# Kernel optimization log

Measured on AMD Instinct MI355X. Metric: run time of the kernel, lower is better.

Reference implementation:

```python
import jax, jax.numpy as jnp
import numpy as np

N_NODES = 20000
N_EDGES = 320000
N_GRAPHS = 64
IN_FEAT = 64
HIDDEN = 256
GRID = 4
NUM_LAYERS = 4  # -> 3 Fourier message-passing layers
NEG_SLOPE = 0.01  # nn.LeakyReLU default


def setup_inputs() -> dict:
    key = jax.random.key(0)
    ks = jax.random.split(key, 8)
    h = jax.random.normal(ks[0], (N_NODES, IN_FEAT), dtype=jnp.float32)
    src = jax.random.randint(ks[1], (N_EDGES,), 0, N_NODES, dtype=jnp.int32)
    dst = jax.random.randint(ks[2], (N_EDGES,), 0, N_NODES, dtype=jnp.int32)
    graph_ids = jnp.sort(jax.random.randint(ks[3], (N_NODES,), 0, N_GRAPHS, dtype=jnp.int32))
    # KAN_polynomial(in_feat, hidden, degree=grid_feat), init randn/(sqrt(in)*sqrt(deg))
    W_line = jax.random.normal(ks[4], (HIDDEN, IN_FEAT, GRID + 1), dtype=jnp.float32) / (
        np.sqrt(IN_FEAT) * np.sqrt(GRID))
    # 3 NaiveFourierKANLayer coeffs [2, out, in, grid]
    fourier_coeffs = jax.random.normal(ks[5], (NUM_LAYERS - 1, 2, HIDDEN, HIDDEN, GRID),
                                       dtype=jnp.float32) / (np.sqrt(HIDDEN) * np.sqrt(GRID))
    # Readout KAN_polynomial(hidden, 1, degree=1, addbias=True)
    W_out = jax.random.normal(ks[6], (1, HIDDEN, 2), dtype=jnp.float32) / np.sqrt(HIDDEN)
    b_out = jnp.zeros((1, 1), dtype=jnp.float32)
    return {"h": h, "src": src, "dst": dst, "graph_ids": graph_ids,
            "W_line": W_line, "fourier_coeffs": fourier_coeffs,
            "W_out": W_out, "b_out": b_out}


def kan_polynomial(x, coeffs, bias=None):
    # x: [b, in], coeffs: [out, in, deg+1]
    deg = coeffs.shape[-1] - 1
    powers = jnp.stack([x ** i for i in range(deg + 1)], axis=-1)  # [b, in, deg+1]
    y = jnp.einsum('bid,oid->bo', powers, coeffs)
    if bias is not None:
        y = y + bias
    return y


def fourier_kan(x, coeffs):
    # x: [N, in], coeffs: [2, out, in, grid]
    grid = coeffs.shape[-1]
    k = jnp.arange(1, grid + 1, dtype=x.dtype)  # [grid]
    ang = x[:, :, None] * k  # [N, in, grid]
    y = jnp.einsum('nig,oig->no', jnp.cos(ang), coeffs[0])
    y = y + jnp.einsum('nig,oig->no', jnp.sin(ang), coeffs[1])
    return y


def reference(h, src, dst, graph_ids, W_line, fourier_coeffs, W_out, b_out):
    # kan_line
    h = kan_polynomial(h, W_line)  # [N, hidden]
    # message-passing Fourier KAN layers with residual + leaky_relu
    for l in range(NUM_LAYERS - 1):
        agg = jax.ops.segment_sum(h[src], dst, num_segments=N_NODES)  # copy_u + sum
        m = fourier_kan(agg, fourier_coeffs[l])
        h = jax.nn.leaky_relu(m + h, negative_slope=NEG_SLOPE)
    # avg pooling per graph
    sums = jax.ops.segment_sum(h, graph_ids, num_segments=N_GRAPHS)  # [G, hidden]
    counts = jax.ops.segment_sum(jnp.ones((N_NODES,), dtype=h.dtype), graph_ids,
                                 num_segments=N_GRAPHS)
    y = sums / jnp.maximum(counts, 1.0)[:, None]
    # Readout: KAN_polynomial(hidden, 1, degree=1) + sigmoid
    out = jax.nn.sigmoid(kan_polynomial(y, W_out, b_out))  # [G, 1]
    return out
```

## Files before the change

kernel.cpp:

```cpp
#include <hip/hip_runtime.h>
#include <math.h>

#define N_NODES   20000
#define N_PAD2    20096
#define N_EDGES   320000
#define N_GRAPHS  64
#define IN_FEAT   64
#define HIDDEN    256
#define GRID_F    4
#define NLAYERS   3
#define NEG_SLOPE 0.01f

#define KF 2048
#define KL4 256
#define NB_SCAN 79
#define NRG  157
#define NBLK (NRG * 4)
#define NLBLK 1256

typedef _Float16 f16x8 __attribute__((ext_vector_type(8)));
typedef _Float16 f16x2 __attribute__((ext_vector_type(2)));
typedef float    f32x4 __attribute__((ext_vector_type(4)));

__global__ void transpose_fourier_f16(const float* __restrict__ fc, _Float16* __restrict__ Bt) {
    int idx = blockIdx.x * 256 + threadIdx.x;
    int kk  = idx & 2047;
    int rest = idx >> 11;
    int o = rest & 255;
    int l = rest >> 8;
    int i = kk >> 3, f = kk & 7, g = f >> 1, t = f & 1;
    Bt[idx] = (_Float16)fc[(((size_t)(l * 2 + t) * HIDDEN + o) * HIDDEN + i) * GRID_F + g];
}

__global__ void transpose_line4(const float* __restrict__ wl, _Float16* __restrict__ Wth,
                                _Float16* __restrict__ Wtl) {
    int idx = blockIdx.x * 256 + threadIdx.x;
    int o = idx >> 8, kk = idx & 255;
    int i = kk >> 2, d = (kk & 3) + 1;
    float wv = wl[(o * IN_FEAT + i) * 5 + d];
    _Float16 h = (_Float16)wv;
    Wth[idx] = h;
    Wtl[idx] = (_Float16)(wv - (float)h);
}

__global__ void line_bias(const float* __restrict__ wl, float* __restrict__ biasv) {
    int o = threadIdx.x;
    float s = 0.f;
    for (int i = 0; i < IN_FEAT; ++i) s += wl[(o * IN_FEAT + i) * 5];
    biasv[o] = s;
}

__global__ void count_deg(const int* __restrict__ dst, int* __restrict__ counts) {
    int e = blockIdx.x * 256 + threadIdx.x;
    if (e < N_EDGES) atomicAdd(&counts[dst[e]], 1);
}

__global__ void block_sums(const int* __restrict__ counts, int* __restrict__ bsum) {
    int i = blockIdx.x * 256 + threadIdx.x;
    int v = (i < N_NODES) ? counts[i] : 0;
    #pragma unroll
    for (int o = 32; o > 0; o >>= 1) v += __shfl_down(v, o, 64);
    __shared__ int ws[4];
    if ((threadIdx.x & 63) == 0) ws[threadIdx.x >> 6] = v;
    __syncthreads();
    if (threadIdx.x == 0) bsum[blockIdx.x] = ws[0] + ws[1] + ws[2] + ws[3];
}

__global__ void scan_mid(const int* __restrict__ bsum, int* __restrict__ bofs,
                         int* __restrict__ row_start) {
    __shared__ int buf[128];
    int t = threadIdx.x;
    int v = (t < NB_SCAN) ? bsum[t] : 0;
    buf[t] = v;
    __syncthreads();
    for (int d = 1; d < 128; d <<= 1) {
        int x = (t >= d) ? buf[t - d] : 0;
        __syncthreads();
        buf[t] += x;
        __syncthreads();
    }
    if (t < NB_SCAN) bofs[t] = buf[t] - v;
    if (t == NB_SCAN - 1) row_start[N_NODES] = buf[t];
}

__global__ void scan_blocks(const int* __restrict__ counts, const int* __restrict__ bofs,
                            int* __restrict__ row_start) {
    int i = blockIdx.x * 256 + threadIdx.x;
    int val = (i < N_NODES) ? counts[i] : 0;
    int lane = threadIdx.x & 63, wid = threadIdx.x >> 6;
    int v = val;
    #pragma unroll
    for (int d = 1; d < 64; d <<= 1) {
        int t = __shfl_up(v, d, 64);
        if (lane >= d) v += t;
    }
    __shared__ int ws[4];
    if (lane == 63) ws[wid] = v;
    __syncthreads();
    int wofs = 0;
    for (int j = 0; j < wid; ++j) wofs += ws[j];
    if (i < N_NODES) row_start[i] = bofs[blockIdx.x] + wofs + v - val;
}

__global__ void fill_csr(const int* __restrict__ src, const int* __restrict__ dst,
                         const int* __restrict__ row_start, int* __restrict__ cursor,
                         int* __restrict__ ssrc) {
    int e = blockIdx.x * 256 + threadIdx.x;
    if (e < N_EDGES) {
        int d = dst[e];
        int pos = row_start[d] + atomicAdd(&cursor[d], 1);
        ssrc[pos] = src[e];
    }
}

__global__ __launch_bounds__(256)
void aggregate(const float* __restrict__ h, const int* __restrict__ row_start,
               const int* __restrict__ ssrc, unsigned* __restrict__ cs) {
    const int node = blockIdx.x * 4 + (threadIdx.x >> 6);
    const int lane = threadIdx.x & 63;
    const int b = row_start[node], e = row_start[node + 1];
    f32x4 a0 = {0.f, 0.f, 0.f, 0.f}, a1 = {0.f, 0.f, 0.f, 0.f};
    int j = b;
    for (; j + 1 < e; j += 2) {
        int s0 = ssrc[j], s1 = ssrc[j + 1];
        a0 += *(const f32x4*)&h[(size_t)s0 * HIDDEN + lane * 4];
        a1 += *(const f32x4*)&h[(size_t)s1 * HIDDEN + lane * 4];
    }
    if (j < e) {
        int s0 = ssrc[j];
        a0 += *(const f32x4*)&h[(size_t)s0 * HIDDEN + lane * 4];
    }
    f32x4 v = a0 + a1;
    unsigned csv[4];
    #pragma unroll
    for (int k = 0; k < 4; ++k) {
        float r = v[k] * 0.15915494309189535f;
        r -= floorf(r);
        _Float16 ch = (_Float16)__builtin_amdgcn_cosf(r);
        _Float16 sh = (_Float16)__builtin_amdgcn_sinf(r);
        union { f16x2 z; unsigned u; } p;
        p.z = (f16x2){ch, sh};
        csv[k] = p.u;
    }
    *(uint4*)&cs[(size_t)node * HIDDEN + lane * 4] = make_uint4(csv[0], csv[1], csv[2], csv[3]);
}

__device__ __forceinline__ void makepow(float xa, float xb, f16x8& hi, f16x8& lo) {
    float p0 = xa, p1 = xa * xa;
    float p2 = p1 * xa, p3 = p1 * p1;
    float q0 = xb, q1 = xb * xb;
    float q2 = q1 * xb, q3 = q1 * q1;
    float pp[8] = {p0, p1, p2, p3, q0, q1, q2, q3};
    #pragma unroll
    for (int j = 0; j < 8; ++j) {
        _Float16 h = (_Float16)pp[j];
        hi[j] = h;
        lo[j] = (_Float16)(pp[j] - (float)h);
    }
}

__global__ __launch_bounds__(256)
void kan_line_mfma(const float* __restrict__ x, const _Float16* __restrict__ Wth,
                   const _Float16* __restrict__ Wtl, const float* __restrict__ biasv,
                   float* __restrict__ out) {
    __shared__ float    As[64][64];
    __shared__ _Float16 Bsh[64][136];
    __shared__ _Float16 Bsl[64][136];

    const int t = threadIdx.x;
    const int w = t >> 6, l = t & 63, ln = l & 15, quad = l >> 4;
    const int wr = w >> 1, wc = w & 1;

    const int g   = blockIdx.x;
    const int bid = (g & 7) * 157 + (g >> 3);
    const int Mbase = (bid >> 2) * 64;
    const int col0  = (bid & 3) * 64;

    #pragma unroll
    for (int r = 0; r < 4; ++r) {
        int idx = r * 256 + t;
        int row = idx >> 4, p = idx & 15;
        int grow = Mbase + row;
        if (grow > N_NODES - 1) grow = N_NODES - 1;
        f32x4 v = *(const f32x4*)&x[(size_t)grow * IN_FEAT + p * 4];
        *(f32x4*)&As[row][(p * 4) ^ ((row & 7) << 2)] = v;
    }
    const _Float16* WthB = Wth + (size_t)col0 * KL4;
    const _Float16* WtlB = Wtl + (size_t)col0 * KL4;
    #pragma unroll
    for (int r = 0; r < 4; ++r) {
        int idx = r * 256 + t;
        int c = idx >> 4, p = idx & 15;
        *(f16x8*)&Bsh[c][p * 8] = *(const f16x8*)&WthB[(size_t)c * KL4 + p * 8];
        *(f16x8*)&Bsl[c][p * 8] = *(const f16x8*)&WtlB[(size_t)c * KL4 + p * 8];
    }
    f16x8 pbh[4], pbl[4];
    #pragma unroll
    for (int r = 0; r < 4; ++r) {
        int idx = r * 256 + t;
        int c = idx >> 4, p = idx & 15;
        pbh[r] = *(const f16x8*)&WthB[(size_t)c * KL4 + 128 + p * 8];
        pbl[r] = *(const f16x8*)&WtlB[(size_t)c * KL4 + 128 + p * 8];
    }
    __syncthreads();

    f32x4 acc[2][2];
    #pragma unroll
    for (int rt = 0; rt < 2; ++rt)
        #pragma unroll
        for (int ct = 0; ct < 2; ++ct)
            acc[rt][ct] = (f32x4){0.f, 0.f, 0.f, 0.f};

    const int lr0 = wr * 32 + ln;
    const int xsw = (lr0 & 7) << 2;

    #pragma unroll
    for (int half = 0; half < 2; ++half) {
        #pragma unroll
        for (int kcl = 0; kcl < 4; ++kcl) {
            const int kc = half * 4 + kcl;
            const int f0 = kc * 8 + quad * 2;
            float x00 = As[lr0     ][f0 ^ xsw];
            float x01 = As[lr0     ][(f0 + 1) ^ xsw];
            float x10 = As[lr0 + 16][f0 ^ xsw];
            float x11 = As[lr0 + 16][(f0 + 1) ^ xsw];
            f16x8 ah0, al0, ah1, al1;
            makepow(x00, x01, ah0, al0);
            makepow(x10, x11, ah1, al1);
            #pragma unroll
            for (int ct = 0; ct < 2; ++ct) {
                const int bc = wc * 32 + ct * 16 + ln;
                f16x8 bh = *(const f16x8*)&Bsh[bc][kcl * 32 + quad * 8];
                f16x8 bl = *(const f16x8*)&Bsl[bc][kcl * 32 + quad * 8];
                acc[0][ct] = __builtin_amdgcn_mfma_f32_16x16x32_f16(ah0, bh, acc[0][ct], 0, 0, 0);
                acc[0][ct] = __builtin_amdgcn_mfma_f32_16x16x32_f16(al0, bh, acc[0][ct], 0, 0, 0);
                acc[0][ct] = __builtin_amdgcn_mfma_f32_16x16x32_f16(ah0, bl, acc[0][ct], 0, 0, 0);
                acc[1][ct] = __builtin_amdgcn_mfma_f32_16x16x32_f16(ah1, bh, acc[1][ct], 0, 0, 0);
                acc[1][ct] = __builtin_amdgcn_mfma_f32_16x16x32_f16(al1, bh, acc[1][ct], 0, 0, 0);
                acc[1][ct] = __builtin_amdgcn_mfma_f32_16x16x32_f16(ah1, bl, acc[1][ct], 0, 0, 0);
            }
        }
        if (half == 0) {
            __syncthreads();
            #pragma unroll
            for (int r = 0; r < 4; ++r) {
                int idx = r * 256 + t;
                int c = idx >> 4, p = idx & 15;
                *(f16x8*)&Bsh[c][p * 8] = pbh[r];
                *(f16x8*)&Bsl[c][p * 8] = pbl[r];
            }
            __syncthreads();
        }
    }

    #pragma unroll
    for (int rt = 0; rt < 2; ++rt) {
        const int row0 = Mbase + wr * 32 + rt * 16 + quad * 4;
        #pragma unroll
        for (int ct = 0; ct < 2; ++ct) {
            const int col = col0 + wc * 32 + ct * 16 + ln;
            const float bv = biasv[col];
            #pragma unroll
            for (int r = 0; r < 4; ++r) {
                const int row = row0 + r;
                if (row < N_NODES)
                    out[(size_t)row * HIDDEN + col] = acc[rt][ct][r] + bv;
            }
        }
    }
}

__device__ __forceinline__ f16x8 expand4(unsigned csu) {
    union { unsigned u; f16x2 z; } w; w.u = csu;
    f16x2 z1 = w.z;
    f16x2 cc = {z1[0], z1[0]};
    f16x2 ms = {(_Float16)(-z1[1]), z1[1]};
    f16x2 z2 = z1 * cc + (f16x2){z1[1], z1[0]} * ms;
    f16x2 z3 = z2 * cc + (f16x2){z2[1], z2[0]} * ms;
    f16x2 z4 = z3 * cc + (f16x2){z3[1], z3[0]} * ms;
    union { f16x8 v; f16x2 p[4]; } u;
    u.p[0] = z1; u.p[1] = z2; u.p[2] = z3; u.p[3] = z4;
    return u.v;
}

__global__ __launch_bounds__(256)
void fourier_mfma(const unsigned* __restrict__ cs, float* hio,
                  const _Float16* __restrict__ Bt) {
    __shared__ _Float16 Bs[2][64][140];
    __shared__ unsigned As[2][128][17];

    const int t    = threadIdx.x;
    const int w    = t >> 6;
    const int l    = t & 63;
    const int ln   = l & 15;
    const int quad = l >> 4;

    const int g   = blockIdx.x;
    const int xcd = g & 7, ii = g >> 3;
    const int bid = (xcd < 4 ? xcd * 79 : 316 + (xcd - 4) * 78) + ii;
    const int Mbase = (bid >> 2) * 128;
    const int col0  = (bid & 3) * 64;

    const int sc = t >> 4, sp = t & 15;
    const int sr = t >> 2, sq = t & 3;
    const _Float16* bg0 = Bt + (size_t)(col0 + sc) * KF + sp * 8;
    const _Float16* bg1 = bg0 + (size_t)16 * KF;
    const _Float16* bg2 = bg0 + (size_t)32 * KF;
    const _Float16* bg3 = bg0 + (size_t)48 * KF;
    const unsigned* ag0 = cs + (size_t)(Mbase + sr) * HIDDEN + sq * 4;
    const unsigned* ag1 = ag0 + (size_t)64 * HIDDEN;

    f32x4 acc[2][4];
    #pragma unroll
    for (int rt = 0; rt < 2; ++rt)
        #pragma unroll
        for (int ct = 0; ct < 4; ++ct)
            acc[rt][ct] = (f32x4){0.f, 0.f, 0.f, 0.f};

    f16x8 sb0, sb1, sb2, sb3;
    uint4 sa0, sa1;

    sb0 = *(const f16x8*)(bg0);
    sb1 = *(const f16x8*)(bg1);
    sb2 = *(const f16x8*)(bg2);
    sb3 = *(const f16x8*)(bg3);
    sa0 = *(const uint4*)(ag0);
    sa1 = *(const uint4*)(ag1);
    *(f16x8*)&Bs[0][sc     ][sp * 8] = sb0;
    *(f16x8*)&Bs[0][sc + 16][sp * 8] = sb1;
    *(f16x8*)&Bs[0][sc + 32][sp * 8] = sb2;
    *(f16x8*)&Bs[0][sc + 48][sp * 8] = sb3;
    As[0][sr     ][sq * 4 + 0] = sa0.x;
    As[0][sr     ][sq * 4 + 1] = sa0.y;
    As[0][sr     ][sq * 4 + 2] = sa0.z;
    As[0][sr     ][sq * 4 + 3] = sa0.w;
    As[0][sr + 64][sq * 4 + 0] = sa1.x;
    As[0][sr + 64][sq * 4 + 1] = sa1.y;
    As[0][sr + 64][sq * 4 + 2] = sa1.z;
    As[0][sr + 64][sq * 4 + 3] = sa1.w;
    __syncthreads();

    const int lr0 = w * 32 + ln;

    for (int kg = 0; kg < 16; ++kg) {
        const int b = kg & 1;
        if (kg < 15) {
            sb0 = *(const f16x8*)(bg0 + (kg + 1) * 128);
            sb1 = *(const f16x8*)(bg1 + (kg + 1) * 128);
            sb2 = *(const f16x8*)(bg2 + (kg + 1) * 128);
            sb3 = *(const f16x8*)(bg3 + (kg + 1) * 128);
            sa0 = *(const uint4*)(ag0 + (kg + 1) * 16);
            sa1 = *(const uint4*)(ag1 + (kg + 1) * 16);
        }
        #pragma unroll
        for (int kc = 0; kc < 4; ++kc) {
            unsigned cv0 = As[b][lr0     ][kc * 4 + quad];
            unsigned cv1 = As[b][lr0 + 16][kc * 4 + quad];
            f16x8 b0 = *(const f16x8*)&Bs[b][ln     ][kc * 32 + quad * 8];
            f16x8 b1 = *(const f16x8*)&Bs[b][ln + 16][kc * 32 + quad * 8];
            f16x8 b2 = *(const f16x8*)&Bs[b][ln + 32][kc * 32 + quad * 8];
            f16x8 b3 = *(const f16x8*)&Bs[b][ln + 48][kc * 32 + quad * 8];
            f16x8 a0 = expand4(cv0);
            f16x8 a1 = expand4(cv1);
            acc[0][0] = __builtin_amdgcn_mfma_f32_16x16x32_f16(a0, b0, acc[0][0], 0, 0, 0);
            acc[0][1] = __builtin_amdgcn_mfma_f32_16x16x32_f16(a0, b1, acc[0][1], 0, 0, 0);
            acc[0][2] = __builtin_amdgcn_mfma_f32_16x16x32_f16(a0, b2, acc[0][2], 0, 0, 0);
            acc[0][3] = __builtin_amdgcn_mfma_f32_16x16x32_f16(a0, b3, acc[0][3], 0, 0, 0);
            acc[1][0] = __builtin_amdgcn_mfma_f32_16x16x32_f16(a1, b0, acc[1][0], 0, 0, 0);
            acc[1][1] = __builtin_amdgcn_mfma_f32_16x16x32_f16(a1, b1, acc[1][1], 0, 0, 0);
            acc[1][2] = __builtin_amdgcn_mfma_f32_16x16x32_f16(a1, b2, acc[1][2], 0, 0, 0);
            acc[1][3] = __builtin_amdgcn_mfma_f32_16x16x32_f16(a1, b3, acc[1][3], 0, 0, 0);
        }
        if (kg < 15) {
            const int nb = b ^ 1;
            *(f16x8*)&Bs[nb][sc     ][sp * 8] = sb0;
            *(f16x8*)&Bs[nb][sc + 16][sp * 8] = sb1;
            *(f16x8*)&Bs[nb][sc + 32][sp * 8] = sb2;
            *(f16x8*)&Bs[nb][sc + 48][sp * 8] = sb3;
            As[nb][sr     ][sq * 4 + 0] = sa0.x;
            As[nb][sr     ][sq * 4 + 1] = sa0.y;
            As[nb][sr     ][sq * 4 + 2] = sa0.z;
            As[nb][sr     ][sq * 4 + 3] = sa0.w;
            As[nb][sr + 64][sq * 4 + 0] = sa1.x;
            As[nb][sr + 64][sq * 4 + 1] = sa1.y;
            As[nb][sr + 64][sq * 4 + 2] = sa1.z;
            As[nb][sr + 64][sq * 4 + 3] = sa1.w;
        }
        __syncthreads();
    }

    #pragma unroll
    for (int rt = 0; rt < 2; ++rt) {
        const int row0 = Mbase + w * 32 + rt * 16 + quad * 4;
        #pragma unroll
        for (int ct = 0; ct < 4; ++ct) {
            const int col = col0 + ct * 16 + ln;
            #pragma unroll
            for (int r = 0; r < 4; ++r) {
                const int row = row0 + r;
                if (row < N_NODES) {
                    float v = acc[rt][ct][r] + hio[(size_t)row * HIDDEN + col];
                    v = v > 0.f ? v : NEG_SLOPE * v;
                    hio[(size_t)row * HIDDEN + col] = v;
                }
            }
        }
    }
}

__global__ void graph_bounds(const int* __restrict__ gid, int* __restrict__ gstart) {
    int g = threadIdx.x;
    if (g < N_GRAPHS) {
        int lo = 0, hi = N_NODES;
        while (lo < hi) { int mid = (lo + hi) >> 1; if (gid[mid] < g) lo = mid + 1; else hi = mid; }
        gstart[g] = lo;
    } else if (g == N_GRAPHS) {
        gstart[g] = N_NODES;
    }
}

__global__ __launch_bounds__(256)
void pool_seg(const float* __restrict__ h, const int* __restrict__ gid,
              float* __restrict__ pooled) {
    const int c = threadIdx.x;
    const int s = blockIdx.x * 128;
    const int e = min(s + 128, N_NODES);
    float acc = 0.f;
    int g = gid[s];
    for (int n = s; n < e; ++n) {
        int gn = gid[n];
        if (gn != g) {
            atomicAdd(&pooled[g * HIDDEN + c], acc);
            acc = 0.f;
            g = gn;
        }
        acc += h[(size_t)n * HIDDEN + c];
    }
    atomicAdd(&pooled[g * HIDDEN + c], acc);
}

__global__ void readout(const float* __restrict__ pooled, const int* __restrict__ gstart,
                        const float* __restrict__ wout, const float* __restrict__ bout,
                        float* __restrict__ out) {
    int g = blockIdx.x, t = threadIdx.x;
    float cnt = fmaxf((float)(gstart[g + 1] - gstart[g]), 1.f);
    float y = pooled[g * HIDDEN + t] / cnt;
    float term = wout[t * 2 + 0] + wout[t * 2 + 1] * y;
    #pragma unroll
    for (int o = 32; o > 0; o >>= 1) term += __shfl_down(term, o, 64);
    __shared__ float wsum[4];
    if ((t & 63) == 0) wsum[t >> 6] = term;
    __syncthreads();
    if (t == 0) {
        float s = wsum[0] + wsum[1] + wsum[2] + wsum[3] + bout[0];
        out[g] = 1.f / (1.f + expf(-s));
    }
}

extern "C" void kernel_launch(void* const* d_in, const int* in_sizes, int n_in,
                              void* d_out, int out_size, void* d_ws, size_t ws_size,
                              hipStream_t stream) {
    const float* h_in  = (const float*)d_in[0];
    const int*   src   = (const int*)d_in[1];
    const int*   dst   = (const int*)d_in[2];
    const int*   gid   = (const int*)d_in[3];
    const float* wline = (const float*)d_in[4];
    const float* fcoef = (const float*)d_in[5];
    const float* wout  = (const float*)d_in[6];
    const float* bout  = (const float*)d_in[7];
    float* out = (float*)d_out;

    char* ws = (char*)d_ws;
    size_t off = 0;
    auto alloc = [&](size_t bytes) {
        size_t o = off;
        off += (bytes + 255) & ~size_t(255);
        return o;
    };
    float*     hbuf      = (float*)(ws + alloc((size_t)N_PAD2 * HIDDEN * 4));
    unsigned*  csbuf     = (unsigned*)(ws + alloc((size_t)N_PAD2 * HIDDEN * 4));
    _Float16*  BtF16     = (_Float16*)(ws + alloc((size_t)NLAYERS * KF * HIDDEN * 2));
    _Float16*  Wth       = (_Float16*)(ws + alloc((size_t)HIDDEN * KL4 * 2));
    _Float16*  Wtl       = (_Float16*)(ws + alloc((size_t)HIDDEN * KL4 * 2));
    float*     biasv     = (float*)(ws + alloc((size_t)HIDDEN * 4));
    int*       row_start = (int*)(ws + alloc((size_t)(N_NODES + 1) * 4));
    int*       counts    = (int*)(ws + alloc((size_t)N_NODES * 4));
    int*       cursor    = (int*)(ws + alloc((size_t)N_NODES * 4));
    int*       ssrc      = (int*)(ws + alloc((size_t)N_EDGES * 4));
    int*       bsum      = (int*)(ws + alloc((size_t)128 * 4));
    int*       bofs      = (int*)(ws + alloc((size_t)128 * 4));
    int*       gstart    = (int*)(ws + alloc((size_t)(N_GRAPHS + 1) * 4));
    float*     pooled    = (float*)(ws + alloc((size_t)N_GRAPHS * HIDDEN * 4));

    hipMemsetAsync(counts, 0, (size_t)N_NODES * 4, stream);
    hipMemsetAsync(cursor, 0, (size_t)N_NODES * 4, stream);
    hipMemsetAsync(pooled, 0, (size_t)N_GRAPHS * HIDDEN * 4, stream);
    hipMemsetAsync(csbuf + (size_t)N_NODES * HIDDEN, 0,
                   (size_t)(N_PAD2 - N_NODES) * HIDDEN * 4, stream);

    transpose_fourier_f16<<<6144, 256, 0, stream>>>(fcoef, BtF16);
    transpose_line4<<<256, 256, 0, stream>>>(wline, Wth, Wtl);
    line_bias<<<1, 256, 0, stream>>>(wline, biasv);
    count_deg<<<(N_EDGES + 255) / 256, 256, 0, stream>>>(dst, counts);
    block_sums<<<NB_SCAN, 256, 0, stream>>>(counts, bsum);
    scan_mid<<<1, 128, 0, stream>>>(bsum, bofs, row_start);
    scan_blocks<<<NB_SCAN, 256, 0, stream>>>(counts, bofs, row_start);
    fill_csr<<<(N_EDGES + 255) / 256, 256, 0, stream>>>(src, dst, row_start, cursor, ssrc);
    graph_bounds<<<1, 128, 0, stream>>>(gid, gstart);

    kan_line_mfma<<<NLBLK, 256, 0, stream>>>(h_in, Wth, Wtl, biasv, hbuf);

    for (int l = 0; l < NLAYERS; ++l) {
        aggregate<<<N_NODES / 4, 256, 0, stream>>>(hbuf, row_start, ssrc, csbuf);
        fourier_mfma<<<NBLK, 256, 0, stream>>>(csbuf, hbuf,
                                               BtF16 + (size_t)l * KF * HIDDEN);
    }

    pool_seg<<<(N_NODES + 127) / 128, 256, 0, stream>>>(hbuf, gid, pooled);
    readout<<<N_GRAPHS, 256, 0, stream>>>(pooled, gstart, wout, bout, out);
}
```

Baseline: 441.3 us.

## Split aggregation across feature slices with one column per thread

The gather-sum aggregation is repartitioned so that each block covers 8 nodes for one 32-column feature slice, giving each thread a single float column instead of a float4. The grid grows from N/4 to N blocks (bid>>3 picks the node group, bid&7 the slice). The aim is more parallelism and more outstanding loads to hide gather latency. In exchange, each edge index is read 8 times as often, loads become 128-byte half-wave accesses instead of full 1 KB rows, and there are more blocks to launch.

```diff
diff --git a/kernel.cpp b/kernel.cpp
--- a/kernel.cpp
+++ b/kernel.cpp
@@ -116,33 +116,30 @@
 __global__ __launch_bounds__(256)
 void aggregate(const float* __restrict__ h, const int* __restrict__ row_start,
                const int* __restrict__ ssrc, unsigned* __restrict__ cs) {
-    const int node = blockIdx.x * 4 + (threadIdx.x >> 6);
-    const int lane = threadIdx.x & 63;
+    const int bid   = blockIdx.x;
+    const int slice = bid & 7;
+    const int ngrp  = bid >> 3;
+    const int t = threadIdx.x;
+    const int w = t >> 6, l = t & 63;
+    const int half = l >> 5, c = l & 31;
+    const int node = ngrp * 8 + w * 2 + half;
+    const int fcol = slice * 32 + c;
     const int b = row_start[node], e = row_start[node + 1];
-    f32x4 a0 = {0.f, 0.f, 0.f, 0.f}, a1 = {0.f, 0.f, 0.f, 0.f};
+    float a0 = 0.f, a1 = 0.f;
     int j = b;
     for (; j + 1 < e; j += 2) {
         int s0 = ssrc[j], s1 = ssrc[j + 1];
-        a0 += *(const f32x4*)&h[(size_t)s0 * HIDDEN + lane * 4];
-        a1 += *(const f32x4*)&h[(size_t)s1 * HIDDEN + lane * 4];
-    }
-    if (j < e) {
-        int s0 = ssrc[j];
-        a0 += *(const f32x4*)&h[(size_t)s0 * HIDDEN + lane * 4];
-    }
-    f32x4 v = a0 + a1;
-    unsigned csv[4];
-    #pragma unroll
-    for (int k = 0; k < 4; ++k) {
-        float r = v[k] * 0.15915494309189535f;
-        r -= floorf(r);
-        _Float16 ch = (_Float16)__builtin_amdgcn_cosf(r);
-        _Float16 sh = (_Float16)__builtin_amdgcn_sinf(r);
-        union { f16x2 z; unsigned u; } p;
-        p.z = (f16x2){ch, sh};
-        csv[k] = p.u;
-    }
-    *(uint4*)&cs[(size_t)node * HIDDEN + lane * 4] = make_uint4(csv[0], csv[1], csv[2], csv[3]);
+        a0 += h[(size_t)s0 * HIDDEN + fcol];
+        a1 += h[(size_t)s1 * HIDDEN + fcol];
+    }
+    if (j < e) a0 += h[(size_t)ssrc[j] * HIDDEN + fcol];
+    float r = (a0 + a1) * 0.15915494309189535f;
+    r -= floorf(r);
+    _Float16 ch = (_Float16)__builtin_amdgcn_cosf(r);
+    _Float16 sh = (_Float16)__builtin_amdgcn_sinf(r);
+    union { f16x2 z; unsigned u; } p;
+    p.z = (f16x2){ch, sh};
+    cs[(size_t)node * HIDDEN + fcol] = p.u;
 }
 
 __device__ __forceinline__ void makepow(float xa, float xb, f16x8& hi, f16x8& lo) {
@@ -511,7 +508,7 @@
     kan_line_mfma<<<NLBLK, 256, 0, stream>>>(h_in, Wth, Wtl, biasv, hbuf);
 
     for (int l = 0; l < NLAYERS; ++l) {
-        aggregate<<<N_NODES / 4, 256, 0, stream>>>(hbuf, row_start, ssrc, csbuf);
+        aggregate<<<N_NODES, 256, 0, stream>>>(hbuf, row_start, ssrc, csbuf);
         fourier_mfma<<<NBLK, 256, 0, stream>>>(csbuf, hbuf,
                                                BtF16 + (size_t)l * KF * HIDDEN);
     }
```

Result: slower. 474.6 us (+7.6%).
